# Performance work log

Hardware: AMD Instinct MI355X
Metric: run time of the kernel (lower is better)

The kernel has to match this reference:

```python
import jax, jax.numpy as jnp
import numpy as np

NUM_HEADS = 8
GROUPS = 32
EPS = 1e-5


def group_norm(x, gamma, beta):
    # x: [B, C, H, W], normalize over (C/G, H, W) per group
    B, C, H, W = x.shape
    xg = x.reshape(B, GROUPS, -1)
    mu = xg.mean(axis=-1, keepdims=True)
    var = xg.var(axis=-1, keepdims=True)
    xg = (xg - mu) * jax.lax.rsqrt(var + EPS)
    x = xg.reshape(B, C, H, W)
    return x * gamma[None, :, None, None] + beta[None, :, None, None]


def reference(x, w_qkv, w_out, b_out, temperature, g1, beta1, g2, beta2,
              w_mlp1, b_mlp1, w_mlp2, b_mlp2):
    B, C, H, W = x.shape
    hd = C // NUM_HEADS
    N = H * W
    identity = x

    xn = group_norm(x, g1, beta1)
    # 1x1 conv == per-pixel matmul
    qkv = jnp.einsum('oc,bchw->bohw', w_qkv, xn)  # [B, 3C, H, W]
    q, k, v = jnp.split(qkv, 3, axis=1)
    q = q.reshape(B, NUM_HEADS, hd, N)
    k = k.reshape(B, NUM_HEADS, hd, N)
    v = v.reshape(B, NUM_HEADS, hd, N)

    temp = jnp.clip(temperature, 1e-4, 10.0)  # [heads,1,1]
    attn = jnp.einsum('bhdi,bhdj->bhij', q, k) * temp[None]  # [B,h,N,N]
    attn = jax.nn.softmax(attn, axis=-1)  # max-subtract is folded into stable softmax

    out = jnp.einsum('bhdj,bhij->bhdi', v, attn)  # [B,h,hd,N]
    out = out.reshape(B, C, H, W)
    out = jnp.einsum('oc,bchw->bohw', w_out, out) + b_out[None, :, None, None]
    x = identity + out

    y = group_norm(x, g2, beta2)
    h = jnp.einsum('oc,bchw->bohw', w_mlp1, y) + b_mlp1[None, :, None, None]
    h = jax.nn.gelu(h, approximate=False)
    m = jnp.einsum('oc,bchw->bohw', w_mlp2, h) + b_mlp2[None, :, None, None]
    return x + m


def setup_inputs() -> dict:
    key = jax.random.key(0)
    ks = jax.random.split(key, 8)
    C = 256
    B, H, W = 2, 64, 64
    hid = C // 4
    s_in = 1.0 / np.sqrt(C)
    s_hid = 1.0 / np.sqrt(hid)
    return {
        'x': jax.random.normal(ks[0], (B, C, H, W), jnp.float32),
        'w_qkv': jax.random.normal(ks[1], (3 * C, C), jnp.float32) * s_in,
        'w_out': jax.random.normal(ks[2], (C, C), jnp.float32) * s_in,
        'b_out': jnp.zeros((C,), jnp.float32),
        'temperature': jnp.ones((NUM_HEADS, 1, 1), jnp.float32) * (C // NUM_HEADS) ** -0.5,
        'g1': jnp.ones((C,), jnp.float32),
        'beta1': jnp.zeros((C,), jnp.float32),
        'g2': jnp.ones((C,), jnp.float32),
        'beta2': jnp.zeros((C,), jnp.float32),
        'w_mlp1': jax.random.normal(ks[3], (hid, C), jnp.float32) * s_in,
        'b_mlp1': jnp.zeros((hid,), jnp.float32),
        'w_mlp2': jax.random.normal(ks[4], (C, hid), jnp.float32) * s_hid,
        'b_mlp2': jnp.zeros((C,), jnp.float32),
    }
```

## Files before the change

kernel.cpp:

```cpp
#include <hip/hip_runtime.h>
#include <hip/hip_bf16.h>
#include <math.h>

#define NB 2
#define NC 256
#define NHEAD 8
#define HD 32
#define NPIX 4096
#define GEPS 1e-5f
#define NCHUNK 2
#define JLEN (NPIX / NCHUNK)

typedef short bf16x8 __attribute__((ext_vector_type(8)));
typedef float f32x4 __attribute__((ext_vector_type(4)));

typedef __attribute__((address_space(3))) unsigned int lds_u32;
typedef __attribute__((address_space(1))) const unsigned int glb_u32;

union U16x8 { uint4 u4; uint2 u2[2]; unsigned u32[4]; unsigned short us[8]; bf16x8 v; };

__device__ inline unsigned short tobf(float f) {
  union { float f; unsigned u; } c; c.f = f;
  return (unsigned short)((c.u + 0x7FFFu + ((c.u >> 16) & 1u)) >> 16);
}
__device__ inline unsigned packtrunc(float lo, float hi) {
  return __builtin_amdgcn_perm(__float_as_uint(hi), __float_as_uint(lo), 0x07060302u);
}
__device__ inline float geluf(float v) {
  return 0.5f * v * (1.f + erff(v * 0.70710678118654752f));
}

__global__ void detect_kernel(const void* __restrict__ x, int* __restrict__ flag) {
  int lane = threadIdx.x;
  const unsigned short* u = (const unsigned short*)x;
  unsigned short h = u[2 * lane];
  unsigned e = (h >> 7) & 0xFFu;
  int weird = (e < 113u || e > 140u) ? 1 : 0;
  unsigned long long mask = __ballot(weird);
  if (lane == 0) flag[0] = (__popcll(mask) > 16) ? 0 : 1;
}

struct ConvArgs { const void* src[13]; int off[14]; };

__device__ inline float ldsrc(const void* p, int idx, int bf) {
  if (bf) {
    unsigned v = ((const unsigned short*)p)[idx];
    return __uint_as_float(v << 16);
  }
  return ((const float*)p)[idx];
}

__global__ __launch_bounds__(256) void conv_prep_kernel(
    ConvArgs a, float* __restrict__ dstbase, const int* __restrict__ flag,
    int total, unsigned short* __restrict__ wqkv_b, unsigned short* __restrict__ wout_b,
    unsigned short* __restrict__ wm1_b, unsigned short* __restrict__ wm2_b,
    float* __restrict__ qscale, float* __restrict__ part1p) {
  int blk = blockIdx.x, t = threadIdx.x;
  int i = blk * 256 + t;
  int bf = *flag;
  float val = 0.f;
  if (i < total) {
    int s = 0;
    while (i >= a.off[s + 1]) ++s;
    val = ldsrc(a.src[s], i - a.off[s], bf);
    dstbase[i] = val;
  }
  __shared__ float rs[256], rq[256];
  int inx = (blk < 8192);
  rs[t] = inx ? val : 0.f;
  rq[t] = inx ? val * val : 0.f;
  __syncthreads();
  for (int o = 128; o > 0; o >>= 1) {
    if (t < o) { rs[t] += rs[t + o]; rq[t] += rq[t + o]; }
    __syncthreads();
  }
  if (t == 0 && inx) { part1p[blk * 2] = rs[0]; part1p[blk * 2 + 1] = rq[0]; }
  if (i < 196608) wqkv_b[i] = tobf(ldsrc(a.src[1], i, bf));
  else if (i < 262144) wout_b[i - 196608] = tobf(ldsrc(a.src[2], i - 196608, bf));
  else if (i < 278528) wm1_b[i - 262144] = tobf(ldsrc(a.src[9], i - 262144, bf));
  else if (i < 294912) wm2_b[i - 278528] = tobf(ldsrc(a.src[11], i - 278528, bf));
  if (i < 768) {
    if (i < 256) {
      float tc = fminf(fmaxf(ldsrc(a.src[4], i >> 5, bf), 1e-4f), 10.f);
      qscale[i] = tc * 1.4426950408889634f;
    } else qscale[i] = 1.0f;
  }
}

__global__ __launch_bounds__(256) void qkv_fused_kernel(
    const float* __restrict__ x_f, const float* __restrict__ part1p,
    const float* __restrict__ g1, const float* __restrict__ be1,
    const unsigned short* __restrict__ W, const float* __restrict__ qscale,
    unsigned short* __restrict__ qn, unsigned short* __restrict__ kn,
    unsigned short* __restrict__ vs) {
  int t = threadIdx.x;
  int w = t >> 6, lane = t & 63, l16 = lane & 15, quad = lane >> 4;
  int p0 = blockIdx.x * 16;
  int b = p0 >> 12;
  __shared__ float red[32][8][2];
  __shared__ float sm[32], si[32];
  {
    int g = t >> 3, seg = t & 7;
    float s = 0.f, s2 = 0.f;
    const float* pp = part1p + ((size_t)(b * 32 + g) * 128 + seg * 16) * 2;
#pragma unroll
    for (int k = 0; k < 16; ++k) { s += pp[k * 2]; s2 += pp[k * 2 + 1]; }
    red[g][seg][0] = s; red[g][seg][1] = s2;
  }
  __syncthreads();
  if (t < 32) {
    float s = 0.f, s2 = 0.f;
#pragma unroll
    for (int k = 0; k < 8; ++k) { s += red[t][k][0]; s2 += red[t][k][1]; }
    float mean = s * (1.f / 32768.f);
    float var = s2 * (1.f / 32768.f) - mean * mean;
    sm[t] = mean; si[t] = rsqrtf(var + GEPS);
  }
  __syncthreads();
  __shared__ unsigned short Ys[16][264];
  {
    int p = t & 15, cg = t >> 4;
    int n = (p0 & 4095) + p;
    const float* src = x_f + ((size_t)b * NC + cg * 16) * NPIX + n;
    U16x8 lo, hi;
#pragma unroll
    for (int cc = 0; cc < 16; ++cc) {
      int c = cg * 16 + cc;
      int g = c >> 3;
      float gg = g1[c] * si[g];
      float vv = (src[(size_t)cc * NPIX] - sm[g]) * gg + be1[c];
      if (cc < 8) lo.us[cc] = tobf(vv); else hi.us[cc - 8] = tobf(vv);
    }
    *(uint4*)&Ys[p][cg * 16] = lo.u4;
    *(uint4*)&Ys[p][cg * 16 + 8] = hi.u4;
  }
  __syncthreads();
  int ob = blockIdx.y * 384 + w * 96;
  f32x4 acc[6] = {};
#pragma unroll
  for (int k0 = 0; k0 < 256; k0 += 32) {
    U16x8 bfr; bfr.u4 = *(const uint4*)&Ys[l16][k0 + quad * 8];
#pragma unroll
    for (int ot = 0; ot < 6; ++ot) {
      U16x8 af;
      af.u4 = *(const uint4*)(W + (size_t)(ob + ot * 16 + l16) * 256 + k0 + quad * 8);
      acc[ot] = __builtin_amdgcn_mfma_f32_16x16x32_bf16(af.v, bfr.v, acc[ot], 0, 0, 0);
    }
  }
  int n = (p0 & 4095) + l16;
#pragma unroll
  for (int ot = 0; ot < 6; ++ot) {
    int oc = ob + ot * 16 + quad * 4;
    float v[4];
#pragma unroll
    for (int r = 0; r < 4; ++r) v[r] = acc[ot][r] * qscale[oc + r];
    int sec = oc >> 8;
    int c = oc & 255;
    if (sec < 2) {
      int hh = c >> 5, d = c & 31;
      unsigned short* base = sec == 0 ? qn : kn;
      uint2 pk;
      pk.x = (unsigned)tobf(v[0]) | ((unsigned)tobf(v[1]) << 16);
      pk.y = (unsigned)tobf(v[2]) | ((unsigned)tobf(v[3]) << 16);
      *(uint2*)(base + ((size_t)(b * NHEAD + hh) * NPIX + n) * HD + d) = pk;
    } else {
#pragma unroll
      for (int r = 0; r < 4; ++r)
        vs[((size_t)(b * NC + c + r)) * NPIX + n] = tobf(v[r]);
    }
  }
}

__global__ __launch_bounds__(256) void attn6_kernel(
    const unsigned short* __restrict__ qn, const unsigned short* __restrict__ kn,
    const unsigned short* __restrict__ vs, float* __restrict__ pO,
    float* __restrict__ pl) {
  int bx = blockIdx.x;
  int iblk = bx & 63, chunk = bx >> 6;
  int i0 = iblk * 64;
  int jbase = chunk * JLEN;
  int h = blockIdx.y, b = blockIdx.z;
  int bh = b * NHEAD + h;
  int t = threadIdx.x;
  int w = t >> 6, lane = t & 63, l16 = lane & 15, quad = lane >> 4;

  __shared__ unsigned short Kt[2048];
  __shared__ unsigned short Vt[2048];
  __shared__ unsigned short Pl[4][16][72];

  U16x8 qf;
  qf.u4 = *(const uint4*)(qn + ((size_t)bh * NPIX + i0 + w * 16 + l16) * HD + quad * 8);
  U16x8 ones;
#pragma unroll
  for (int j = 0; j < 8; ++j) ones.us[j] = 0x3F80;

  int kj = (w << 4) + (lane >> 2);
  int kg = (lane & 3) ^ ((kj >> 1) & 3);
  const unsigned short* kgp = kn + ((size_t)bh * NPIX + jbase + kj) * HD + kg * 8;
  int vd = (w << 3) + (lane >> 3);
  int vg = (lane & 7) ^ (vd & 7);
  const unsigned short* vgp = vs + ((size_t)(b * NC + h * HD + vd)) * NPIX + jbase + vg * 8;
  lds_u32* kdst = (lds_u32*)&Kt[w * 512];
  lds_u32* vdst = (lds_u32*)&Vt[w * 512];

  f32x4 o0 = {0.f, 0.f, 0.f, 0.f}, o1 = {0.f, 0.f, 0.f, 0.f};
  f32x4 lacc = {0.f, 0.f, 0.f, 0.f};
  const f32x4 zf = {0.f, 0.f, 0.f, 0.f};

  int sp = (quad ^ ((l16 >> 1) & 3)) * 8;
  for (int jt = 0; jt < JLEN; jt += 64) {
    __builtin_amdgcn_global_load_lds((glb_u32*)kgp, kdst, 16, 0, 0);
    __builtin_amdgcn_global_load_lds((glb_u32*)vgp, vdst, 16, 0, 0);
    kgp += 64 * HD;
    vgp += 64;
    __syncthreads();
    f32x4 st[4];
#pragma unroll
    for (int jj = 0; jj < 4; ++jj) {
      U16x8 kf; kf.u4 = *(const uint4*)&Kt[(jj * 16 + l16) * 32 + sp];
      st[jj] = __builtin_amdgcn_mfma_f32_16x16x32_bf16(kf.v, qf.v, zf, 0, 0, 0);
    }
#pragma unroll
    for (int jj = 0; jj < 4; ++jj) {
      uint2 pk;
      pk.x = packtrunc(__builtin_amdgcn_exp2f(st[jj][0]), __builtin_amdgcn_exp2f(st[jj][1]));
      pk.y = packtrunc(__builtin_amdgcn_exp2f(st[jj][2]), __builtin_amdgcn_exp2f(st[jj][3]));
      *(uint2*)&Pl[w][l16][jj * 16 + quad * 4] = pk;
    }
#pragma unroll
    for (int ks = 0; ks < 2; ++ks) {
      U16x8 pb; pb.u4 = *(const uint4*)&Pl[w][l16][ks * 32 + quad * 8];
      int vp = ((ks * 4 + quad) ^ (l16 & 7)) * 8;
      U16x8 va; va.u4 = *(const uint4*)&Vt[l16 * 64 + vp];
      U16x8 vb2; vb2.u4 = *(const uint4*)&Vt[(16 + l16) * 64 + vp];
      o0 = __builtin_amdgcn_mfma_f32_16x16x32_bf16(va.v, pb.v, o0, 0, 0, 0);
      o1 = __builtin_amdgcn_mfma_f32_16x16x32_bf16(vb2.v, pb.v, o1, 0, 0, 0);
      lacc = __builtin_amdgcn_mfma_f32_16x16x32_bf16(ones.v, pb.v, lacc, 0, 0, 0);
    }
    __syncthreads();
  }

  int pr = bh * 64 + iblk;
  float* ob = pO + ((size_t)chunk * 1024 + pr) * 2048;
  int icol = w * 16 + l16;
#pragma unroll
  for (int r = 0; r < 4; ++r) {
    ob[(quad * 4 + r) * 64 + icol] = o0[r];
    ob[(16 + quad * 4 + r) * 64 + icol] = o1[r];
  }
  if (quad == 0)
    pl[((size_t)chunk * 1024 + pr) * 64 + icol] = lacc[0];
}

__global__ __launch_bounds__(256) void attn_combine_kernel(
    const float* __restrict__ pO, const float* __restrict__ pl,
    unsigned short* __restrict__ aout_t) {
  int pr = blockIdx.x;
  int b = pr >> 9, h = (pr >> 6) & 7, iblk = pr & 63;
  int t = threadIdx.x;
  int i = t & 63, dg = t >> 6;
  float l = 0.f;
#pragma unroll
  for (int c = 0; c < NCHUNK; ++c) l += pl[((size_t)c * 1024 + pr) * 64 + i];
  float rinv = 1.f / l;
  U16x8 pk;
#pragma unroll
  for (int dd = 0; dd < 8; ++dd) {
    int d = dg * 8 + dd;
    float v = 0.f;
#pragma unroll
    for (int c = 0; c < NCHUNK; ++c)
      v += pO[((size_t)c * 1024 + pr) * 2048 + d * 64 + i];
    pk.us[dd] = tobf(v * rinv);
  }
  *(uint4*)(aout_t + ((size_t)b * NPIX + iblk * 64 + i) * NC + h * 32 + dg * 8) = pk.u4;
}

__global__ __launch_bounds__(256) void wout_kernel(
    const unsigned short* __restrict__ W, const unsigned short* __restrict__ X,
    const float* __restrict__ bias, const float* __restrict__ res,
    float* __restrict__ xres, float* __restrict__ part2p) {
  int t = threadIdx.x;
  int w = t >> 6, lane = t & 63, l16 = lane & 15, quad = lane >> 4;
  int p = blockIdx.x * 16 + l16;
  int ob = w * 64;
  const unsigned short* xrow = X + (size_t)p * 256 + quad * 8;
  f32x4 acc[4] = {};
#pragma unroll
  for (int k0 = 0; k0 < 256; k0 += 32) {
    U16x8 bfr; bfr.u4 = *(const uint4*)(xrow + k0);
#pragma unroll
    for (int ot = 0; ot < 4; ++ot) {
      U16x8 af;
      af.u4 = *(const uint4*)(W + (size_t)(ob + ot * 16 + l16) * 256 + k0 + quad * 8);
      acc[ot] = __builtin_amdgcn_mfma_f32_16x16x32_bf16(af.v, bfr.v, acc[ot], 0, 0, 0);
    }
  }
  int b = p >> 12, n = p & 4095;
  __shared__ float sb[256][4][2];
#pragma unroll
  for (int ot = 0; ot < 4; ++ot) {
    int oc = ob + ot * 16 + quad * 4;
    float s = 0.f, s2 = 0.f;
#pragma unroll
    for (int r = 0; r < 4; ++r) {
      size_t oidx = ((size_t)(b * NC + oc + r)) * NPIX + n;
      float vv = acc[ot][r] + bias[oc + r] + res[oidx];
      xres[oidx] = vv;
      s += vv; s2 += vv * vv;
    }
    sb[t][ot][0] = s; sb[t][ot][1] = s2;
  }
  __syncthreads();
  if (t < 32) {
    int ww = t >> 3, rem = t & 7, ot = rem >> 1, qp = rem & 1;
    float s = 0.f, s2 = 0.f;
#pragma unroll
    for (int q = 2 * qp; q < 2 * qp + 2; ++q)
      for (int l = 0; l < 16; ++l) {
        int tt = ww * 64 + q * 16 + l;
        s += sb[tt][ot][0]; s2 += sb[tt][ot][1];
      }
    size_t idx = ((size_t)(b * 32 + t) * 256 + (blockIdx.x & 255)) * 2;
    part2p[idx] = s; part2p[idx + 1] = s2;
  }
}

__global__ __launch_bounds__(256) void mlp_fused_kernel(
    const float* __restrict__ xres, const float* __restrict__ part2p,
    const float* __restrict__ g2, const float* __restrict__ be2,
    const unsigned short* __restrict__ W1, const float* __restrict__ b1,
    const unsigned short* __restrict__ W2, const float* __restrict__ b2,
    void* __restrict__ dout, const int* __restrict__ flag) {
  int t = threadIdx.x;
  int w = t >> 6, lane = t & 63, l16 = lane & 15, quad = lane >> 4;
  int p0 = blockIdx.x * 16;
  int b = p0 >> 12;
  __shared__ float red[32][8][2];
  __shared__ float sm[32], si[32];
  {
    int g = t >> 3, seg = t & 7;
    float s = 0.f, s2 = 0.f;
    const float* pp = part2p + ((size_t)(b * 32 + g) * 256 + seg * 32) * 2;
#pragma unroll
    for (int k = 0; k < 32; ++k) { s += pp[k * 2]; s2 += pp[k * 2 + 1]; }
    red[g][seg][0] = s; red[g][seg][1] = s2;
  }
  __syncthreads();
  if (t < 32) {
    float s = 0.f, s2 = 0.f;
#pragma unroll
    for (int k = 0; k < 8; ++k) { s += red[t][k][0]; s2 += red[t][k][1]; }
    float mean = s * (1.f / 32768.f);
    float var = s2 * (1.f / 32768.f) - mean * mean;
    sm[t] = mean; si[t] = rsqrtf(var + GEPS);
  }
  __syncthreads();
  __shared__ float Xs[16][261];
  __shared__ unsigned short Ys[16][264];
  {
    int p = t & 15, cg = t >> 4;
    int n = (p0 & 4095) + p;
    const float* src = xres + ((size_t)b * NC + cg * 16) * NPIX + n;
    U16x8 lo, hi;
#pragma unroll
    for (int cc = 0; cc < 16; ++cc) {
      int c = cg * 16 + cc;
      int g = c >> 3;
      float v = src[(size_t)cc * NPIX];
      Xs[p][c] = v;
      float yv = (v - sm[g]) * (g2[c] * si[g]) + be2[c];
      if (cc < 8) lo.us[cc] = tobf(yv); else hi.us[cc - 8] = tobf(yv);
    }
    *(uint4*)&Ys[p][cg * 16] = lo.u4;
    *(uint4*)&Ys[p][cg * 16 + 8] = hi.u4;
  }
  __syncthreads();
  f32x4 a1 = {0.f, 0.f, 0.f, 0.f};
#pragma unroll
  for (int k0 = 0; k0 < 256; k0 += 32) {
    U16x8 bfr; bfr.u4 = *(const uint4*)&Ys[l16][k0 + quad * 8];
    U16x8 af;
    af.u4 = *(const uint4*)(W1 + (size_t)(w * 16 + l16) * 256 + k0 + quad * 8);
    a1 = __builtin_amdgcn_mfma_f32_16x16x32_bf16(af.v, bfr.v, a1, 0, 0, 0);
  }
  __shared__ unsigned short Hs[16][72];
  {
    int oc = w * 16 + quad * 4;
    float h0 = geluf(a1[0] + b1[oc]),     h1 = geluf(a1[1] + b1[oc + 1]);
    float h2 = geluf(a1[2] + b1[oc + 2]), h3 = geluf(a1[3] + b1[oc + 3]);
    uint2 pk;
    pk.x = (unsigned)tobf(h0) | ((unsigned)tobf(h1) << 16);
    pk.y = (unsigned)tobf(h2) | ((unsigned)tobf(h3) << 16);
    *(uint2*)&Hs[l16][oc] = pk;
  }
  __syncthreads();
  f32x4 a2[4] = {};
#pragma unroll
  for (int k0 = 0; k0 < 64; k0 += 32) {
    U16x8 bfr; bfr.u4 = *(const uint4*)&Hs[l16][k0 + quad * 8];
#pragma unroll
    for (int ot = 0; ot < 4; ++ot) {
      U16x8 af;
      af.u4 = *(const uint4*)(W2 + (size_t)(w * 64 + ot * 16 + l16) * 64 + k0 + quad * 8);
      a2[ot] = __builtin_amdgcn_mfma_f32_16x16x32_bf16(af.v, bfr.v, a2[ot], 0, 0, 0);
    }
  }
  int n = (p0 & 4095) + l16;
  int wbf = *flag;
#pragma unroll
  for (int ot = 0; ot < 4; ++ot) {
    int oc = w * 64 + ot * 16 + quad * 4;
#pragma unroll
    for (int r = 0; r < 4; ++r) {
      float v = a2[ot][r] + b2[oc + r] + Xs[l16][oc + r];
      size_t oidx = ((size_t)(b * NC + oc + r)) * NPIX + n;
      if (wbf) ((__hip_bfloat16*)dout)[oidx] = __float2bfloat16(v);
      else ((float*)dout)[oidx] = v;
    }
  }
}

extern "C" void kernel_launch(void* const* d_in, const int* in_sizes, int n_in,
                              void* d_out, int out_size, void* d_ws, size_t ws_size,
                              hipStream_t stream) {
  float* ws = (float*)d_ws;
  int* flag = (int*)d_ws;
  size_t off = 16;
  float* x_f    = ws + off; off += (size_t)NB * NC * NPIX;
  float* wqkv_f = ws + off; off += 768 * 256;
  float* wout_f = ws + off; off += 256 * 256;
  float* bout_f = ws + off; off += 256;
  float* temp_f = ws + off; off += 8;
  float* g1_f   = ws + off; off += 256;
  float* be1_f  = ws + off; off += 256;
  float* g2_f   = ws + off; off += 256;
  float* be2_f  = ws + off; off += 256;
  float* wm1_f  = ws + off; off += 64 * 256;
  float* bm1_f  = ws + off; off += 64;
  float* wm2_f  = ws + off; off += 256 * 64;
  float* bm2_f  = ws + off; off += 256;
  float* xres   = ws + off; off += (size_t)NB * NC * NPIX;
  unsigned short* qn     = (unsigned short*)(ws + off); off += 1048576;
  unsigned short* kn     = (unsigned short*)(ws + off); off += 1048576;
  unsigned short* vs     = (unsigned short*)(ws + off); off += 1048576;
  unsigned short* aout_t = (unsigned short*)(ws + off); off += 1048576;
  unsigned short* wqkv_b = (unsigned short*)(ws + off); off += 98304;
  unsigned short* wout_b = (unsigned short*)(ws + off); off += 32768;
  unsigned short* wm1_b  = (unsigned short*)(ws + off); off += 8192;
  unsigned short* wm2_b  = (unsigned short*)(ws + off); off += 8192;
  float* qscale = ws + off; off += 768;
  float* part1p = ws + off; off += 16384;
  float* part2p = ws + off; off += 65536;
  float* pO     = ws + off; off += (size_t)NCHUNK * 1024 * 2048;
  float* plb    = ws + off; off += (size_t)NCHUNK * 1024 * 64;
  (void)wqkv_f; (void)wout_f; (void)wm1_f; (void)wm2_f; (void)temp_f; (void)bm1_f;

  detect_kernel<<<1, 64, 0, stream>>>(d_in[0], flag);

  ConvArgs ca;
  int acc = 0;
  for (int i = 0; i < 13; ++i) {
    ca.src[i] = d_in[i];
    ca.off[i] = acc;
    acc += (i < n_in) ? in_sizes[i] : 0;
  }
  ca.off[13] = acc;
  conv_prep_kernel<<<(acc + 255) / 256, 256, 0, stream>>>(
      ca, x_f, flag, acc, wqkv_b, wout_b, wm1_b, wm2_b, qscale, part1p);

  qkv_fused_kernel<<<dim3(512, 2), 256, 0, stream>>>(
      x_f, part1p, g1_f, be1_f, wqkv_b, qscale, qn, kn, vs);

  attn6_kernel<<<dim3(64 * NCHUNK, NHEAD, NB), 256, 0, stream>>>(qn, kn, vs, pO, plb);
  attn_combine_kernel<<<1024, 256, 0, stream>>>(pO, plb, aout_t);

  wout_kernel<<<512, 256, 0, stream>>>(wout_b, aout_t, bout_f, x_f, xres, part2p);

  mlp_fused_kernel<<<512, 256, 0, stream>>>(
      xres, part2p, g2_f, be2_f, wm1_b, bm1_f, wm2_b, bm2_f, d_out, flag);
}
```

Before: 226.6 us.

## Fuse attention combine into out-projection, double-buffer K, inline dtype detection

Removes the separate attn_combine kernel: the output-projection kernel now sums the two chunk partials, divides by the summed softmax denominator, and packs to bf16 on the fly. The attention kernel double-buffers K tiles in LDS, loads V fragments directly from global memory into registers, and drops one barrier per iteration. The dtype-detection kernel is folded into the prep and MLP kernels as a per-block check. This saves two launches and one intermediate buffer round trip, but the out-projection now does strided fp32 gathers and the V loads are no longer staged through LDS.

```diff
diff --git a/kernel.cpp b/kernel.cpp
--- a/kernel.cpp
+++ b/kernel.cpp
@@ -30,14 +30,18 @@
   return 0.5f * v * (1.f + erff(v * 0.70710678118654752f));
 }
 
-__global__ void detect_kernel(const void* __restrict__ x, int* __restrict__ flag) {
-  int lane = threadIdx.x;
-  const unsigned short* u = (const unsigned short*)x;
-  unsigned short h = u[2 * lane];
-  unsigned e = (h >> 7) & 0xFFu;
-  int weird = (e < 113u || e > 140u) ? 1 : 0;
-  unsigned long long mask = __ballot(weird);
-  if (lane == 0) flag[0] = (__popcll(mask) > 16) ? 0 : 1;
+__device__ inline int detect_bf(const void* xraw) {
+  __shared__ int flg;
+  int t = threadIdx.x;
+  if (t < 64) {
+    unsigned short h = ((const unsigned short*)xraw)[2 * t];
+    unsigned e = (h >> 7) & 0xFFu;
+    int weird = (e < 113u || e > 140u) ? 1 : 0;
+    unsigned long long m = __ballot(weird);
+    if (t == 0) flg = (__popcll(m) > 16) ? 0 : 1;
+  }
+  __syncthreads();
+  return flg;
 }
 
 struct ConvArgs { const void* src[13]; int off[14]; };
@@ -51,13 +55,13 @@
 }
 
 __global__ __launch_bounds__(256) void conv_prep_kernel(
-    ConvArgs a, float* __restrict__ dstbase, const int* __restrict__ flag,
-    int total, unsigned short* __restrict__ wqkv_b, unsigned short* __restrict__ wout_b,
+    ConvArgs a, float* __restrict__ dstbase, int total,
+    unsigned short* __restrict__ wqkv_b, unsigned short* __restrict__ wout_b,
     unsigned short* __restrict__ wm1_b, unsigned short* __restrict__ wm2_b,
     float* __restrict__ qscale, float* __restrict__ part1p) {
+  int bf = detect_bf(a.src[0]);
   int blk = blockIdx.x, t = threadIdx.x;
   int i = blk * 256 + t;
-  int bf = *flag;
   float val = 0.f;
   if (i < total) {
     int s = 0;
@@ -171,7 +175,7 @@
   }
 }
 
-__global__ __launch_bounds__(256) void attn6_kernel(
+__global__ __launch_bounds__(256) void attn7_kernel(
     const unsigned short* __restrict__ qn, const unsigned short* __restrict__ kn,
     const unsigned short* __restrict__ vs, float* __restrict__ pO,
     float* __restrict__ pl) {
@@ -184,8 +188,7 @@
   int t = threadIdx.x;
   int w = t >> 6, lane = t & 63, l16 = lane & 15, quad = lane >> 4;
 
-  __shared__ unsigned short Kt[2048];
-  __shared__ unsigned short Vt[2048];
+  __shared__ unsigned short Kt[2][2048];
   __shared__ unsigned short Pl[4][16][72];
 
   U16x8 qf;
@@ -197,27 +200,36 @@
   int kj = (w << 4) + (lane >> 2);
   int kg = (lane & 3) ^ ((kj >> 1) & 3);
   const unsigned short* kgp = kn + ((size_t)bh * NPIX + jbase + kj) * HD + kg * 8;
-  int vd = (w << 3) + (lane >> 3);
-  int vg = (lane & 7) ^ (vd & 7);
-  const unsigned short* vgp = vs + ((size_t)(b * NC + h * HD + vd)) * NPIX + jbase + vg * 8;
-  lds_u32* kdst = (lds_u32*)&Kt[w * 512];
-  lds_u32* vdst = (lds_u32*)&Vt[w * 512];
+  const unsigned short* vrow0 = vs + ((size_t)(b * NC + h * HD + l16)) * NPIX + jbase + quad * 8;
+  const unsigned short* vrow1 = vrow0 + (size_t)16 * NPIX;
 
   f32x4 o0 = {0.f, 0.f, 0.f, 0.f}, o1 = {0.f, 0.f, 0.f, 0.f};
   f32x4 lacc = {0.f, 0.f, 0.f, 0.f};
   const f32x4 zf = {0.f, 0.f, 0.f, 0.f};
 
+  __builtin_amdgcn_global_load_lds((glb_u32*)kgp, (lds_u32*)&Kt[0][w * 512], 16, 0, 0);
+  kgp += 64 * HD;
+
   int sp = (quad ^ ((l16 >> 1) & 3)) * 8;
-  for (int jt = 0; jt < JLEN; jt += 64) {
-    __builtin_amdgcn_global_load_lds((glb_u32*)kgp, kdst, 16, 0, 0);
-    __builtin_amdgcn_global_load_lds((glb_u32*)vgp, vdst, 16, 0, 0);
-    kgp += 64 * HD;
-    vgp += 64;
+  const int NT = JLEN / 64;
+  for (int it = 0; it < NT; ++it) {
+    int cur = it & 1;
     __syncthreads();
+    if (it + 1 < NT) {
+      __builtin_amdgcn_global_load_lds((glb_u32*)kgp, (lds_u32*)&Kt[cur ^ 1][w * 512], 16, 0, 0);
+      kgp += 64 * HD;
+    }
+    int j0 = it * 64;
+    U16x8 vf0[2], vf1[2];
+#pragma unroll
+    for (int ks = 0; ks < 2; ++ks) {
+      vf0[ks].u4 = *(const uint4*)(vrow0 + j0 + ks * 32);
+      vf1[ks].u4 = *(const uint4*)(vrow1 + j0 + ks * 32);
+    }
     f32x4 st[4];
 #pragma unroll
     for (int jj = 0; jj < 4; ++jj) {
-      U16x8 kf; kf.u4 = *(const uint4*)&Kt[(jj * 16 + l16) * 32 + sp];
+      U16x8 kf; kf.u4 = *(const uint4*)&Kt[cur][(jj * 16 + l16) * 32 + sp];
       st[jj] = __builtin_amdgcn_mfma_f32_16x16x32_bf16(kf.v, qf.v, zf, 0, 0, 0);
     }
 #pragma unroll
@@ -230,14 +242,10 @@
 #pragma unroll
     for (int ks = 0; ks < 2; ++ks) {
       U16x8 pb; pb.u4 = *(const uint4*)&Pl[w][l16][ks * 32 + quad * 8];
-      int vp = ((ks * 4 + quad) ^ (l16 & 7)) * 8;
-      U16x8 va; va.u4 = *(const uint4*)&Vt[l16 * 64 + vp];
-      U16x8 vb2; vb2.u4 = *(const uint4*)&Vt[(16 + l16) * 64 + vp];
-      o0 = __builtin_amdgcn_mfma_f32_16x16x32_bf16(va.v, pb.v, o0, 0, 0, 0);
-      o1 = __builtin_amdgcn_mfma_f32_16x16x32_bf16(vb2.v, pb.v, o1, 0, 0, 0);
+      o0 = __builtin_amdgcn_mfma_f32_16x16x32_bf16(vf0[ks].v, pb.v, o0, 0, 0, 0);
+      o1 = __builtin_amdgcn_mfma_f32_16x16x32_bf16(vf1[ks].v, pb.v, o1, 0, 0, 0);
       lacc = __builtin_amdgcn_mfma_f32_16x16x32_bf16(ones.v, pb.v, lacc, 0, 0, 0);
     }
-    __syncthreads();
   }
 
   int pr = bh * 64 + iblk;
@@ -252,43 +260,38 @@
     pl[((size_t)chunk * 1024 + pr) * 64 + icol] = lacc[0];
 }
 
-__global__ __launch_bounds__(256) void attn_combine_kernel(
-    const float* __restrict__ pO, const float* __restrict__ pl,
-    unsigned short* __restrict__ aout_t) {
-  int pr = blockIdx.x;
-  int b = pr >> 9, h = (pr >> 6) & 7, iblk = pr & 63;
-  int t = threadIdx.x;
-  int i = t & 63, dg = t >> 6;
-  float l = 0.f;
-#pragma unroll
-  for (int c = 0; c < NCHUNK; ++c) l += pl[((size_t)c * 1024 + pr) * 64 + i];
-  float rinv = 1.f / l;
-  U16x8 pk;
-#pragma unroll
-  for (int dd = 0; dd < 8; ++dd) {
-    int d = dg * 8 + dd;
-    float v = 0.f;
-#pragma unroll
-    for (int c = 0; c < NCHUNK; ++c)
-      v += pO[((size_t)c * 1024 + pr) * 2048 + d * 64 + i];
-    pk.us[dd] = tobf(v * rinv);
-  }
-  *(uint4*)(aout_t + ((size_t)b * NPIX + iblk * 64 + i) * NC + h * 32 + dg * 8) = pk.u4;
-}
-
 __global__ __launch_bounds__(256) void wout_kernel(
-    const unsigned short* __restrict__ W, const unsigned short* __restrict__ X,
-    const float* __restrict__ bias, const float* __restrict__ res,
-    float* __restrict__ xres, float* __restrict__ part2p) {
+    const unsigned short* __restrict__ W, const float* __restrict__ pO,
+    const float* __restrict__ pl, const float* __restrict__ bias,
+    const float* __restrict__ res, float* __restrict__ xres,
+    float* __restrict__ part2p) {
   int t = threadIdx.x;
   int w = t >> 6, lane = t & 63, l16 = lane & 15, quad = lane >> 4;
   int p = blockIdx.x * 16 + l16;
+  int b = p >> 12, n = p & 4095;
+  int i = p & 63, iblk = (p >> 6) & 63;
   int ob = w * 64;
-  const unsigned short* xrow = X + (size_t)p * 256 + quad * 8;
+  float rinv8[8];
+#pragma unroll
+  for (int hh = 0; hh < 8; ++hh) {
+    size_t pr = (size_t)(b * NHEAD + hh) * 64 + iblk;
+    float l = pl[pr * 64 + i] + pl[(1024 + pr) * 64 + i];
+    rinv8[hh] = 1.f / l;
+  }
   f32x4 acc[4] = {};
 #pragma unroll
   for (int k0 = 0; k0 < 256; k0 += 32) {
-    U16x8 bfr; bfr.u4 = *(const uint4*)(xrow + k0);
+    int hh = k0 >> 5;
+    const float* q0 = pO + ((size_t)(b * NHEAD + hh) * 64 + iblk) * 2048 + quad * 8 * 64 + i;
+    const float* q1 = q0 + (size_t)1024 * 2048;
+    float rv = rinv8[hh];
+    U16x8 bfr;
+#pragma unroll
+    for (int u = 0; u < 4; ++u) {
+      float va = (q0[(2 * u) * 64] + q1[(2 * u) * 64]) * rv;
+      float vb = (q0[(2 * u + 1) * 64] + q1[(2 * u + 1) * 64]) * rv;
+      bfr.u32[u] = packtrunc(va, vb);
+    }
 #pragma unroll
     for (int ot = 0; ot < 4; ++ot) {
       U16x8 af;
@@ -296,7 +299,6 @@
       acc[ot] = __builtin_amdgcn_mfma_f32_16x16x32_bf16(af.v, bfr.v, acc[ot], 0, 0, 0);
     }
   }
-  int b = p >> 12, n = p & 4095;
   __shared__ float sb[256][4][2];
 #pragma unroll
   for (int ot = 0; ot < 4; ++ot) {
@@ -327,11 +329,12 @@
 }
 
 __global__ __launch_bounds__(256) void mlp_fused_kernel(
-    const float* __restrict__ xres, const float* __restrict__ part2p,
-    const float* __restrict__ g2, const float* __restrict__ be2,
-    const unsigned short* __restrict__ W1, const float* __restrict__ b1,
-    const unsigned short* __restrict__ W2, const float* __restrict__ b2,
-    void* __restrict__ dout, const int* __restrict__ flag) {
+    const void* __restrict__ xraw, const float* __restrict__ xres,
+    const float* __restrict__ part2p, const float* __restrict__ g2,
+    const float* __restrict__ be2, const unsigned short* __restrict__ W1,
+    const float* __restrict__ b1, const unsigned short* __restrict__ W2,
+    const float* __restrict__ b2, void* __restrict__ dout) {
+  int wbf = detect_bf(xraw);
   int t = threadIdx.x;
   int w = t >> 6, lane = t & 63, l16 = lane & 15, quad = lane >> 4;
   int p0 = blockIdx.x * 16;
@@ -407,7 +410,6 @@
     }
   }
   int n = (p0 & 4095) + l16;
-  int wbf = *flag;
 #pragma unroll
   for (int ot = 0; ot < 4; ++ot) {
     int oc = w * 64 + ot * 16 + quad * 4;
@@ -425,7 +427,6 @@
                               void* d_out, int out_size, void* d_ws, size_t ws_size,
                               hipStream_t stream) {
   float* ws = (float*)d_ws;
-  int* flag = (int*)d_ws;
   size_t off = 16;
   float* x_f    = ws + off; off += (size_t)NB * NC * NPIX;
   float* wqkv_f = ws + off; off += 768 * 256;
@@ -444,7 +445,6 @@
   unsigned short* qn     = (unsigned short*)(ws + off); off += 1048576;
   unsigned short* kn     = (unsigned short*)(ws + off); off += 1048576;
   unsigned short* vs     = (unsigned short*)(ws + off); off += 1048576;
-  unsigned short* aout_t = (unsigned short*)(ws + off); off += 1048576;
   unsigned short* wqkv_b = (unsigned short*)(ws + off); off += 98304;
   unsigned short* wout_b = (unsigned short*)(ws + off); off += 32768;
   unsigned short* wm1_b  = (unsigned short*)(ws + off); off += 8192;
@@ -456,8 +456,6 @@
   float* plb    = ws + off; off += (size_t)NCHUNK * 1024 * 64;
   (void)wqkv_f; (void)wout_f; (void)wm1_f; (void)wm2_f; (void)temp_f; (void)bm1_f;
 
-  detect_kernel<<<1, 64, 0, stream>>>(d_in[0], flag);
-
   ConvArgs ca;
   int acc = 0;
   for (int i = 0; i < 13; ++i) {
@@ -467,16 +465,15 @@
   }
   ca.off[13] = acc;
   conv_prep_kernel<<<(acc + 255) / 256, 256, 0, stream>>>(
-      ca, x_f, flag, acc, wqkv_b, wout_b, wm1_b, wm2_b, qscale, part1p);
+      ca, x_f, acc, wqkv_b, wout_b, wm1_b, wm2_b, qscale, part1p);
 
   qkv_fused_kernel<<<dim3(512, 2), 256, 0, stream>>>(
       x_f, part1p, g1_f, be1_f, wqkv_b, qscale, qn, kn, vs);
 
-  attn6_kernel<<<dim3(64 * NCHUNK, NHEAD, NB), 256, 0, stream>>>(qn, kn, vs, pO, plb);
-  attn_combine_kernel<<<1024, 256, 0, stream>>>(pO, plb, aout_t);
-
-  wout_kernel<<<512, 256, 0, stream>>>(wout_b, aout_t, bout_f, x_f, xres, part2p);
+  attn7_kernel<<<dim3(64 * NCHUNK, NHEAD, NB), 256, 0, stream>>>(qn, kn, vs, pO, plb);
+
+  wout_kernel<<<512, 256, 0, stream>>>(wout_b, pO, plb, bout_f, x_f, xres, part2p);
 
   mlp_fused_kernel<<<512, 256, 0, stream>>>(
-      xres, part2p, g2_f, be2_f, wm1_b, bm1_f, wm2_b, bm2_f, d_out, flag);
-}
+      d_in[0], xres, part2p, g2_f, be2_f, wm1_b, bm1_f, wm2_b, bm2_f, d_out);
+}
```

Result: slower. 289.4 us (+27.7%).
